# Kernel tuning notes

Hardware: AMD Instinct MI355X
Metric: run time of the kernel (lower is better)

## Reference

```python
import jax, jax.numpy as jnp
import numpy as np

B, S, F, E, D = 64, 64, 512, 1024, 1024

def setup_inputs() -> dict:
    key = jax.random.key(0)
    k1, k2, k3, k4, k5 = jax.random.split(key, 5)
    sen_emb = jax.random.normal(k1, (B, S, E), dtype=jnp.float32)
    features = jax.random.normal(k2, (B, F, D), dtype=jnp.float32)
    # lengths in [1, F] so softmax always has at least one valid element
    feature_lens = jax.random.randint(k3, (B,), 1, F + 1, dtype=jnp.int64)
    W = jax.random.normal(k4, (E + D,), dtype=jnp.float32) * (1.0 / np.sqrt(E + D))
    b = jax.random.normal(k5, (1,), dtype=jnp.float32) * 0.01
    return {"sen_emb": sen_emb, "features": features, "feature_lens": feature_lens, "W": W, "b": b}

def reference(sen_emb, features, feature_lens, W, b):
    E_ = sen_emb.shape[-1]
    W_e, W_f = W[:E_], W[E_:]
    # additive score decomposes: Linear(cat(e, f)) = e.W_e + f.W_f + b
    s_emb = jnp.einsum('bse,e->bs', sen_emb, W_e)          # [B, S]
    s_ftr = jnp.einsum('bfd,d->bf', features, W_f)          # [B, F]
    scores = s_emb[:, :, None] + s_ftr[:, None, :] + b[0]   # [B, S, F]
    valid = jnp.arange(features.shape[1])[None, :] < feature_lens[:, None]  # [B, F]
    neg = jnp.finfo(scores.dtype).min
    scores = jnp.where(valid[:, None, :], scores, neg)
    attn = jax.nn.softmax(scores, axis=-1)                  # [B, S, F]
    return jnp.einsum('bsf,bfd->bsd', attn, features)       # [B, S, D]
```

## Files before the change

kernel.cpp:

```cpp
#include <hip/hip_runtime.h>
#include <cfloat>

#define B_ 64
#define S_ 64
#define F_ 512
#define E_ 1024
#define D_ 1024
#define FT_ 32
#define NT_ (F_ / FT_)

__global__ __launch_bounds__(256) void k_rowdot(const float* __restrict__ features,
                                                const float* __restrict__ W_f,
                                                const int* __restrict__ lens,
                                                float* __restrict__ s_ftr) {
    const int wave = threadIdx.x >> 6;
    const int lane = threadIdx.x & 63;
    const int row  = blockIdx.x * 4 + wave;
    const int b    = row >> 9;
    const int f    = row & (F_ - 1);
    if (f >= lens[b]) return;

    const float4* fp = reinterpret_cast<const float4*>(features + (size_t)row * D_);
    const float4* wp = reinterpret_cast<const float4*>(W_f);
    float acc = 0.f;
#pragma unroll
    for (int j = 0; j < 4; ++j) {
        const float4 v = fp[lane + 64 * j];
        const float4 w = wp[lane + 64 * j];
        acc = fmaf(v.x, w.x, acc);
        acc = fmaf(v.y, w.y, acc);
        acc = fmaf(v.z, w.z, acc);
        acc = fmaf(v.w, w.w, acc);
    }
#pragma unroll
    for (int off = 32; off; off >>= 1) acc += __shfl_xor(acc, off, 64);
    if (lane == 0) s_ftr[row] = acc;
}

__global__ __launch_bounds__(256) void k_ctx_part(const float* __restrict__ features,
                                                  const float* __restrict__ s_ftr,
                                                  const int* __restrict__ lens,
                                                  float* __restrict__ part) {
    const int b    = blockIdx.y;
    const int tile = blockIdx.x;
    const int len  = lens[b];
    const int f0   = tile * FT_;
    if (f0 >= len) return;

    __shared__ float sw[F_];
    __shared__ float red_m[4], red_s[4];
    const int t    = threadIdx.x;
    const int wave = t >> 6;
    const int lane = t & 63;

    const float v0 = (t       < len) ? s_ftr[b * F_ + t]       : -FLT_MAX;
    const float v1 = (t + 256 < len) ? s_ftr[b * F_ + t + 256] : -FLT_MAX;
    float m = fmaxf(v0, v1);
#pragma unroll
    for (int off = 32; off; off >>= 1) m = fmaxf(m, __shfl_xor(m, off, 64));
    if (lane == 0) red_m[wave] = m;
    __syncthreads();
    const float m4 = fmaxf(fmaxf(red_m[0], red_m[1]), fmaxf(red_m[2], red_m[3]));

    const float e0 = (t       < len) ? __expf(v0 - m4) : 0.f;
    const float e1 = (t + 256 < len) ? __expf(v1 - m4) : 0.f;
    float s = e0 + e1;
#pragma unroll
    for (int off = 32; off; off >>= 1) s += __shfl_xor(s, off, 64);
    if (lane == 0) red_s[wave] = s;
    __syncthreads();
    const float inv = 1.f / (red_s[0] + red_s[1] + red_s[2] + red_s[3]);
    sw[t]       = e0 * inv;
    sw[t + 256] = e1 * inv;
    __syncthreads();

    const float4* fb = reinterpret_cast<const float4*>(features + ((size_t)b * F_ + f0) * D_);
    float4 acc = make_float4(0.f, 0.f, 0.f, 0.f);
    const int nf = min(FT_, len - f0);
    for (int f = 0; f < nf; ++f) {
        const float  w = sw[f0 + f];
        const float4 v = fb[f * 256 + t];
        acc.x = fmaf(w, v.x, acc.x);
        acc.y = fmaf(w, v.y, acc.y);
        acc.z = fmaf(w, v.z, acc.z);
        acc.w = fmaf(w, v.w, acc.w);
    }
    reinterpret_cast<float4*>(part)[((size_t)b * NT_ + tile) * 256 + t] = acc;
}

__global__ __launch_bounds__(256) void k_bcast(const float* __restrict__ part,
                                               const int* __restrict__ lens,
                                               float* __restrict__ out) {
    const int b  = blockIdx.y;
    const int t  = threadIdx.x;
    const int nt = min(NT_, (lens[b] + FT_ - 1) / FT_);

    const float4* pp = reinterpret_cast<const float4*>(part) + (size_t)b * NT_ * 256 + t;
    float4 acc = make_float4(0.f, 0.f, 0.f, 0.f);
    for (int k = 0; k < nt; ++k) {
        const float4 v = pp[(size_t)k * 256];
        acc.x += v.x; acc.y += v.y; acc.z += v.z; acc.w += v.w;
    }

    const int s0 = blockIdx.x * 8;
    float4* ob = reinterpret_cast<float4*>(out) + ((size_t)b * S_ + s0) * 256 + t;
#pragma unroll
    for (int s = 0; s < 8; ++s) ob[(size_t)s * 256] = acc;
}

extern "C" void kernel_launch(void* const* d_in, const int* in_sizes, int n_in,
                              void* d_out, int out_size, void* d_ws, size_t ws_size,
                              hipStream_t stream) {
    (void)in_sizes; (void)n_in; (void)out_size; (void)ws_size;
    const float* features = (const float*)d_in[1];
    const int*   lens     = (const int*)d_in[2];
    const float* W        = (const float*)d_in[3];
    float*       out      = (float*)d_out;

    float* s_ftr = (float*)d_ws;
    float* part  = s_ftr + B_ * F_;

    k_rowdot  <<<dim3(B_ * F_ / 4), 256, 0, stream>>>(features, W + E_, lens, s_ftr);
    k_ctx_part<<<dim3(NT_, B_),     256, 0, stream>>>(features, s_ftr, lens, part);
    k_bcast   <<<dim3(8, B_),       256, 0, stream>>>(part, lens, out);
}
```

Baseline: 209.5 us.

## Fuse row-dot scoring into context kernel with split-softmax combine

Merges the score-computing row-dot kernel into the per-tile context kernel, so each tile computes its own scores, a local max and sum, and an unnormalized weighted feature sum, in the style of flash attention. A combine kernel rescales the partial results using the per-tile max and sum to recover the exact softmax. This drops one kernel launch and the global round trip of the score array. Features in each tile are read twice by the same block (once for scores, once for the weighted sum), and the second read is expected to hit cache. The change also cuts the per-block parallelism available for the scoring phase.

```diff
diff --git a/kernel.cpp b/kernel.cpp
--- a/kernel.cpp
+++ b/kernel.cpp
@@ -9,98 +9,104 @@
 #define FT_ 32
 #define NT_ (F_ / FT_)
 
-__global__ __launch_bounds__(256) void k_rowdot(const float* __restrict__ features,
-                                                const float* __restrict__ W_f,
-                                                const int* __restrict__ lens,
-                                                float* __restrict__ s_ftr) {
-    const int wave = threadIdx.x >> 6;
-    const int lane = threadIdx.x & 63;
-    const int row  = blockIdx.x * 4 + wave;
-    const int b    = row >> 9;
-    const int f    = row & (F_ - 1);
-    if (f >= lens[b]) return;
-
-    const float4* fp = reinterpret_cast<const float4*>(features + (size_t)row * D_);
-    const float4* wp = reinterpret_cast<const float4*>(W_f);
-    float acc = 0.f;
-#pragma unroll
-    for (int j = 0; j < 4; ++j) {
-        const float4 v = fp[lane + 64 * j];
-        const float4 w = wp[lane + 64 * j];
-        acc = fmaf(v.x, w.x, acc);
-        acc = fmaf(v.y, w.y, acc);
-        acc = fmaf(v.z, w.z, acc);
-        acc = fmaf(v.w, w.w, acc);
-    }
-#pragma unroll
-    for (int off = 32; off; off >>= 1) acc += __shfl_xor(acc, off, 64);
-    if (lane == 0) s_ftr[row] = acc;
-}
-
-__global__ __launch_bounds__(256) void k_ctx_part(const float* __restrict__ features,
-                                                  const float* __restrict__ s_ftr,
-                                                  const int* __restrict__ lens,
-                                                  float* __restrict__ part) {
+__global__ __launch_bounds__(256) void k_flash(const float* __restrict__ features,
+                                               const float* __restrict__ W_f,
+                                               const int* __restrict__ lens,
+                                               float* __restrict__ part,
+                                               float* __restrict__ mbuf,
+                                               float* __restrict__ sbuf) {
     const int b    = blockIdx.y;
     const int tile = blockIdx.x;
     const int len  = lens[b];
     const int f0   = tile * FT_;
     if (f0 >= len) return;
+    const int nf   = min(FT_, len - f0);
 
-    __shared__ float sw[F_];
-    __shared__ float red_m[4], red_s[4];
+    __shared__ float s_row[FT_];
+    __shared__ float sw[FT_];
     const int t    = threadIdx.x;
     const int wave = t >> 6;
     const int lane = t & 63;
 
-    const float v0 = (t       < len) ? s_ftr[b * F_ + t]       : -FLT_MAX;
-    const float v1 = (t + 256 < len) ? s_ftr[b * F_ + t + 256] : -FLT_MAX;
-    float m = fmaxf(v0, v1);
+    const float4* fb = reinterpret_cast<const float4*>(features + ((size_t)b * F_ + f0) * D_);
+    const float4* wp = reinterpret_cast<const float4*>(W_f);
+
+    for (int f = wave; f < FT_; f += 4) {
+        float acc;
+        if (f < nf) {
+            acc = 0.f;
 #pragma unroll
-    for (int off = 32; off; off >>= 1) m = fmaxf(m, __shfl_xor(m, off, 64));
-    if (lane == 0) red_m[wave] = m;
-    __syncthreads();
-    const float m4 = fmaxf(fmaxf(red_m[0], red_m[1]), fmaxf(red_m[2], red_m[3]));
-
-    const float e0 = (t       < len) ? __expf(v0 - m4) : 0.f;
-    const float e1 = (t + 256 < len) ? __expf(v1 - m4) : 0.f;
-    float s = e0 + e1;
+            for (int j = 0; j < 4; ++j) {
+                const float4 v = fb[(size_t)f * 256 + lane + 64 * j];
+                const float4 w = wp[lane + 64 * j];
+                acc = fmaf(v.x, w.x, acc);
+                acc = fmaf(v.y, w.y, acc);
+                acc = fmaf(v.z, w.z, acc);
+                acc = fmaf(v.w, w.w, acc);
+            }
 #pragma unroll
-    for (int off = 32; off; off >>= 1) s += __shfl_xor(s, off, 64);
-    if (lane == 0) red_s[wave] = s;
-    __syncthreads();
-    const float inv = 1.f / (red_s[0] + red_s[1] + red_s[2] + red_s[3]);
-    sw[t]       = e0 * inv;
-    sw[t + 256] = e1 * inv;
+            for (int off = 32; off; off >>= 1) acc += __shfl_xor(acc, off, 64);
+        } else {
+            acc = -FLT_MAX;
+        }
+        if (lane == 0) s_row[f] = acc;
+    }
     __syncthreads();
 
-    const float4* fb = reinterpret_cast<const float4*>(features + ((size_t)b * F_ + f0) * D_);
+    float m = -FLT_MAX;
+#pragma unroll
+    for (int f = 0; f < FT_; ++f) m = fmaxf(m, s_row[f]);
+    if (t < FT_) sw[t] = (t < nf) ? __expf(s_row[t] - m) : 0.f;
+    __syncthreads();
+    float ssum = 0.f;
+#pragma unroll
+    for (int f = 0; f < FT_; ++f) ssum += sw[f];
+
     float4 acc = make_float4(0.f, 0.f, 0.f, 0.f);
-    const int nf = min(FT_, len - f0);
     for (int f = 0; f < nf; ++f) {
-        const float  w = sw[f0 + f];
-        const float4 v = fb[f * 256 + t];
+        const float  w = sw[f];
+        const float4 v = fb[(size_t)f * 256 + t];
         acc.x = fmaf(w, v.x, acc.x);
         acc.y = fmaf(w, v.y, acc.y);
         acc.z = fmaf(w, v.z, acc.z);
         acc.w = fmaf(w, v.w, acc.w);
     }
     reinterpret_cast<float4*>(part)[((size_t)b * NT_ + tile) * 256 + t] = acc;
+    if (t == 0) {
+        mbuf[b * NT_ + tile] = m;
+        sbuf[b * NT_ + tile] = ssum;
+    }
 }
 
-__global__ __launch_bounds__(256) void k_bcast(const float* __restrict__ part,
-                                               const int* __restrict__ lens,
-                                               float* __restrict__ out) {
+__global__ __launch_bounds__(256) void k_combine(const float* __restrict__ part,
+                                                 const float* __restrict__ mbuf,
+                                                 const float* __restrict__ sbuf,
+                                                 const int* __restrict__ lens,
+                                                 float* __restrict__ out) {
     const int b  = blockIdx.y;
     const int t  = threadIdx.x;
     const int nt = min(NT_, (lens[b] + FT_ - 1) / FT_);
 
+    __shared__ float fac[NT_];
+    float M = -FLT_MAX;
+    for (int k = 0; k < nt; ++k) M = fmaxf(M, mbuf[b * NT_ + k]);
+    if (t < NT_) fac[t] = (t < nt) ? __expf(mbuf[b * NT_ + t] - M) : 0.f;
+    __syncthreads();
+    float S = 0.f;
+    for (int k = 0; k < nt; ++k) S += fac[k] * sbuf[b * NT_ + k];
+    const float inv = 1.f / S;
+
     const float4* pp = reinterpret_cast<const float4*>(part) + (size_t)b * NT_ * 256 + t;
     float4 acc = make_float4(0.f, 0.f, 0.f, 0.f);
     for (int k = 0; k < nt; ++k) {
+        const float  f = fac[k];
         const float4 v = pp[(size_t)k * 256];
-        acc.x += v.x; acc.y += v.y; acc.z += v.z; acc.w += v.w;
+        acc.x = fmaf(f, v.x, acc.x);
+        acc.y = fmaf(f, v.y, acc.y);
+        acc.z = fmaf(f, v.z, acc.z);
+        acc.w = fmaf(f, v.w, acc.w);
     }
+    acc.x *= inv; acc.y *= inv; acc.z *= inv; acc.w *= inv;
 
     const int s0 = blockIdx.x * 8;
     float4* ob = reinterpret_cast<float4*>(out) + ((size_t)b * S_ + s0) * 256 + t;
@@ -117,10 +123,10 @@
     const float* W        = (const float*)d_in[3];
     float*       out      = (float*)d_out;
 
-    float* s_ftr = (float*)d_ws;
-    float* part  = s_ftr + B_ * F_;
+    float* part = (float*)d_ws;
+    float* mbuf = part + (size_t)B_ * NT_ * D_;
+    float* sbuf = mbuf + B_ * NT_;
 
-    k_rowdot  <<<dim3(B_ * F_ / 4), 256, 0, stream>>>(features, W + E_, lens, s_ftr);
-    k_ctx_part<<<dim3(NT_, B_),     256, 0, stream>>>(features, s_ftr, lens, part);
-    k_bcast   <<<dim3(8, B_),       256, 0, stream>>>(part, lens, out);
+    k_flash  <<<dim3(NT_, B_), 256, 0, stream>>>(features, W + E_, lens, part, mbuf, sbuf);
+    k_combine<<<dim3(8, B_),   256, 0, stream>>>(part, mbuf, sbuf, lens, out);
 }
```

After: 210.5 us. Within noise of the previous version (+0.5%).
